# Kernel tuning notes

Hardware: AMD Instinct MI355X
Metric: run time of the kernel (lower is better)

The kernel has to match this reference:

```python
import jax, jax.numpy as jnp
import numpy as np

N_QUBITS = 6
N_LAYERS = 2
QSVT_DEGREE = 3
BATCH = 128
SEQ_LEN = 512
DIM = 2 ** N_QUBITS
# wire 0 is the most-significant bit in the statevector index (PennyLane convention)
_POP = np.array([bin(i).count('1') for i in range(DIM)], dtype=np.float32)
PHASE_SIGN = jnp.asarray(N_QUBITS - 2.0 * _POP)  # (DIM,): sum_w (1 - 2*bit_w)


def _rx(t):
    c = jnp.cos(0.5 * t).astype(jnp.complex64)
    s = (-1j * jnp.sin(0.5 * t)).astype(jnp.complex64)
    return jnp.stack([jnp.stack([c, s]), jnp.stack([s, c])])


def _ry(t):
    c = jnp.cos(0.5 * t).astype(jnp.complex64)
    s = jnp.sin(0.5 * t).astype(jnp.complex64)
    return jnp.stack([jnp.stack([c, -s]), jnp.stack([s, c])])


def _rz(t):
    e = jnp.exp(-0.5j * t.astype(jnp.complex64))
    z = jnp.zeros((), jnp.complex64)
    return jnp.stack([jnp.stack([e, z]), jnp.stack([z, jnp.conj(e)])])


def _apply_1q(psi, U, w):
    # psi: (B,) + (2,)*N_QUBITS ; U: (2,2) complex, same for all batch elems
    psi = jnp.moveaxis(psi, 1 + w, -1)
    psi = psi @ U.T
    return jnp.moveaxis(psi, -1, 1 + w)


def _apply_ry_batched(psi, theta, w):
    # RY with a per-batch angle theta: (B,)
    psi = jnp.moveaxis(psi, 1 + w, -1)
    c = jnp.cos(0.5 * theta).reshape((-1,) + (1,) * (N_QUBITS - 1))
    s = jnp.sin(0.5 * theta).reshape((-1,) + (1,) * (N_QUBITS - 1))
    a, b = psi[..., 0], psi[..., 1]
    psi = jnp.stack([c * a - s * b, s * a + c * b], axis=-1)
    return jnp.moveaxis(psi, -1, 1 + w)


def _cnot(psi, c, t):
    p0 = jax.lax.index_in_dim(psi, 0, axis=1 + c, keepdims=True)
    p1 = jax.lax.index_in_dim(psi, 1, axis=1 + c, keepdims=True)
    p1 = jnp.flip(p1, axis=1 + t)
    return jnp.concatenate([p0, p1], axis=1 + c)


def _circuit_step(h, x, params, poly):
    # h, x: (B, N_QUBITS) angles. Returns <Z_w> per qubit: (B, N_QUBITS).
    B = h.shape[0]
    # 1) state encoding: RY(h_w)|0> = cos(h/2)|0> + sin(h/2)|1>  (product state)
    c, s = jnp.cos(0.5 * h), jnp.sin(0.5 * h)
    psi = jnp.ones((B, 1), jnp.complex64)
    for w in range(N_QUBITS):
        amp = jnp.stack([c[:, w], s[:, w]], axis=-1).astype(jnp.complex64)  # (B,2)
        psi = (psi[:, :, None] * amp[:, None, :]).reshape(B, -1)
    psi = psi.reshape((B,) + (2,) * N_QUBITS)
    # 2) QSVT block: RZ(coeff*pi) on every wire fuses into one diagonal phase
    for d in range(QSVT_DEGREE + 1):
        theta = poly[d] * np.pi
        phase = jnp.exp((-0.5j) * theta * PHASE_SIGN)  # (DIM,)
        psi = (psi.reshape(B, -1) * phase[None, :]).reshape((B,) + (2,) * N_QUBITS)
        for i in range(N_QUBITS - 1):
            psi = _cnot(psi, i, i + 1)
        psi = _cnot(psi, N_QUBITS - 1, 0)  # ring closure
    # 3) variational layers: per-wire RZ@RY@RX (RX applied first), then CNOT chain
    idx = 0
    for _ in range(N_LAYERS):
        for i in range(N_QUBITS):
            U = _rz(params[idx + 2]) @ _ry(params[idx + 1]) @ _rx(params[idx])
            psi = _apply_1q(psi, U, i)
            idx += 3
        for i in range(N_QUBITS - 1):
            psi = _cnot(psi, i, i + 1)
    # 4) input injection: RY(x_w) with per-batch angles
    for w in range(N_QUBITS):
        psi = _apply_ry_batched(psi, x[:, w], w)
    # 5) measurement: <Z_w> = P(bit_w=0) - P(bit_w=1)
    p = jnp.abs(psi) ** 2
    zs = []
    for w in range(N_QUBITS):
        axes = tuple(a for a in range(1, N_QUBITS + 1) if a != 1 + w)
        pw = p.sum(axis=axes)  # (B,2)
        zs.append(pw[:, 0] - pw[:, 1])
    return jnp.stack(zs, axis=-1)


def _ssm_pass(angles, params, poly, reverse):
    a = jnp.flip(angles, axis=1) if reverse else angles
    xs = jnp.moveaxis(a, 1, 0)  # (T, B, n)
    h0 = jnp.zeros((a.shape[0], N_QUBITS), jnp.float32)

    def step(h, x):
        hn = _circuit_step(h, x, params, poly)
        return hn, hn

    _, ys = jax.lax.scan(step, h0, xs)
    out = jnp.moveaxis(ys, 0, 1)  # (B, T, n)
    return jnp.flip(out, axis=1) if reverse else out


def setup_inputs() -> dict:
    key = jax.random.key(0)
    k0, k1, k2, k3 = jax.random.split(key, 4)
    angles = jax.random.uniform(k0, (BATCH, SEQ_LEN, N_QUBITS), jnp.float32) * np.float32(np.pi)
    poly_coeffs = jax.random.normal(k1, (QSVT_DEGREE + 1,), jnp.float32) * 0.1
    fwd_params = jax.random.normal(k2, (N_QUBITS * N_LAYERS * 3,), jnp.float32) * 0.1
    bwd_params = jax.random.normal(k3, (N_QUBITS * N_LAYERS * 3,), jnp.float32) * 0.1
    fwd_coeff = jnp.full((1,), 0.5, jnp.float32)
    bwd_coeff = jnp.full((1,), 0.5, jnp.float32)
    return {'angles': angles, 'poly_coeffs': poly_coeffs, 'fwd_params': fwd_params,
            'bwd_params': bwd_params, 'fwd_coeff': fwd_coeff, 'bwd_coeff': bwd_coeff}


def reference(angles, poly_coeffs, fwd_params, bwd_params, fwd_coeff, bwd_coeff):
    h_fwd = _ssm_pass(angles, fwd_params, poly_coeffs, reverse=False)
    h_bwd = _ssm_pass(angles, bwd_params, poly_coeffs, reverse=True)
    return jax.nn.sigmoid(fwd_coeff) * h_fwd + jax.nn.sigmoid(bwd_coeff) * h_bwd
```

## Files before the change

kernel.cpp:

```cpp
#include <hip/hip_runtime.h>
#include <hip/hip_bf16.h>
#include <stdint.h>

#define BATCH 128
#define SEQ   512
#define NW    6
#define DIM   64
#define NELEM (BATCH * SEQ * NW)
#define PI_F  3.14159265358979323846f

typedef float v2f __attribute__((ext_vector_type(2)));
typedef uint16_t u16x8 __attribute__((ext_vector_type(8)));

__device__ __forceinline__ v2f pkfma(float s, v2f m, v2f a) {
    return __builtin_elementwise_fma((v2f){s, s}, m, a);
}

template <int CTRL>
__device__ __forceinline__ float dpp_mov(float x) {
    return __int_as_float(__builtin_amdgcn_update_dpp(
        0, __float_as_int(x), CTRL, 0xF, 0xF, false));
}

template <int CTRL>
__device__ __forceinline__ float dpp_add(float v) {
    return v + __int_as_float(__builtin_amdgcn_update_dpp(
        0, __float_as_int(v), CTRL, 0xF, 0xF, true));
}

__device__ __forceinline__ float swap16_add(float v) {
    auto r = __builtin_amdgcn_permlane16_swap(
        __float_as_int(v), __float_as_int(v), false, false);
    return __int_as_float((int)r[0]) + __int_as_float((int)r[1]);
}
__device__ __forceinline__ float swap32_add(float v) {
    auto r = __builtin_amdgcn_permlane32_swap(
        __float_as_int(v), __float_as_int(v), false, false);
    return __int_as_float((int)r[0]) + __int_as_float((int)r[1]);
}

__device__ __forceinline__ void sincos_half(float h, float& s, float& c) {
    const float u = h * h;
    c = fmaf(u, fmaf(u, 2.6041667e-3f, -0.125f), 1.0f);
    s = h * fmaf(u, fmaf(u, 2.6041667e-4f, -2.0833333e-2f), 0.5f);
}

__device__ __forceinline__ float ldf(const void* p, int i, bool bf) {
    if (bf) {
        uint32_t u = (uint32_t)((const uint16_t*)p)[i];
        return __uint_as_float(u << 16);
    }
    return ((const float*)p)[i];
}

__global__ void k_prep(const void* ang, const void* poly, const void* fp,
                       const void* bp, const void* fc, const void* bc,
                       float* __restrict__ misc, float* __restrict__ Mg,
                       int* __restrict__ flag) {
    __shared__ int cnt;
    if (threadIdx.x == 0) cnt = 0;
    __syncthreads();
    {
        uint32_t w = ((const uint32_t*)ang)[threadIdx.x & 255];
        uint32_t e = (w >> 8) & 0xFFu;
        if (e >= 0x3Au && e <= 0x41u) atomicAdd(&cnt, 1);
    }
    __syncthreads();
    const bool bf = (cnt >= 128);

    if (blockIdx.x == 32) {
        if (threadIdx.x == 0)      misc[76] = ldf(fc, 0, bf);
        else if (threadIdx.x == 1) misc[77] = ldf(bc, 0, bf);
        else if (threadIdx.x == 2) *flag = bf ? 1 : 0;
        return;
    }

    const int lane = threadIdx.x & 63;
    const int tix  = blockIdx.x * 4 + (threadIdx.x >> 6);
    const int dir  = tix >> 6;
    const int col  = tix & 63;
    const void* prm = dir ? bp : fp;
    const int p = lane;

    float yr = (p == col) ? 1.f : 0.f;
    float yi = 0.f;

#pragma unroll
    for (int d = 0; d < 4; ++d) {
        const float th = 0.5f * PI_F * ldf(poly, d, bf) *
                         (float)(6 - 2 * (int)__popc((unsigned)p));
        float s, c;
        __sincosf(th, &s, &c);
        const float nr = yr * c + yi * s;
        const float ni = yi * c - yr * s;
        yr = nr; yi = ni;
#pragma unroll
        for (int k = 0; k < 6; ++k) {
            const int cw = k, tw = (k + 1) % 6;
            const int src = p ^ (((p >> (5 - cw)) & 1) << (5 - tw));
            yr = __shfl(yr, src, 64);
            yi = __shfl(yi, src, 64);
        }
    }

    int idx = 0;
#pragma unroll
    for (int l = 0; l < 2; ++l) {
#pragma unroll
        for (int w = 0; w < 6; ++w) {
            float cx, sx, cy, sy, cz, sz;
            __sincosf(0.5f * ldf(prm, idx + 0, bf), &sx, &cx);
            __sincosf(0.5f * ldf(prm, idx + 1, bf), &sy, &cy);
            __sincosf(0.5f * ldf(prm, idx + 2, bf), &sz, &cz);
            idx += 3;
            const float A = cy * cx, B = sy * sx, C = sy * cx, D = cy * sx;
            const float U00r = cz * A + sz * B, U00i = cz * B - sz * A;
            const float U11r = U00r,            U11i = sz * A - cz * B;
            const float Xr   = cz * C + sz * D, Xi   = sz * C - cz * D;
            const int m  = 1 << (5 - w);
            const int bb = (p >> (5 - w)) & 1;
            const float C1r = bb ? U11r : U00r;
            const float C1i = bb ? U11i : U00i;
            const float C2r = bb ? Xr : -Xr;
            const float C2i = Xi;
            const float pr = __shfl_xor(yr, m, 64);
            const float pi = __shfl_xor(yi, m, 64);
            const float nr = C1r * yr - C1i * yi + C2r * pr - C2i * pi;
            const float ni = C1r * yi + C1i * yr + C2r * pi + C2i * pr;
            yr = nr; yi = ni;
        }
#pragma unroll
        for (int k = 0; k < 5; ++k) {
            const int src = p ^ (((p >> (5 - k)) & 1) << (5 - (k + 1)));
            yr = __shfl(yr, src, 64);
            yi = __shfl(yi, src, 64);
        }
    }

    float* out = Mg + ((size_t)(dir * 64 + p) * 64 + (size_t)col) * 2;
    out[0] = yr;
    out[1] = yi;
}

__global__ void __launch_bounds__(256, 1) k_sim(const void* __restrict__ ang,
                                                const float* __restrict__ Mg,
                                                float* __restrict__ hbuf,
                                                const int* __restrict__ flag) {
    const int tid   = threadIdx.x;
    const int lane  = tid & 63;
    const int wv    = tid >> 6;
    const int chain = blockIdx.x;
    const int dir   = chain >> 7;
    const int b     = chain & 127;
    const bool bf   = (*flag != 0);

    __shared__ __align__(16) float  cl[SEQ * 12];
    __shared__ __align__(16) float  zb[SEQ * NW];
    __shared__ float2 pY[2][4][DIM];

    if (!bf) {
        const float4* src =
            (const float4*)((const float*)ang + (size_t)b * (SEQ * NW));
#pragma unroll
        for (int k = 0; k < 3; ++k) {
            const int v = k * 256 + tid;
            const float4 a = src[v];
            __align__(16) float o[8];
            float s, c;
            __sincosf(a.x, &s, &c); o[0] = c; o[1] = s;
            __sincosf(a.y, &s, &c); o[2] = c; o[3] = s;
            __sincosf(a.z, &s, &c); o[4] = c; o[5] = s;
            __sincosf(a.w, &s, &c); o[6] = c; o[7] = s;
            ((float4*)cl)[2 * v]     = ((const float4*)o)[0];
            ((float4*)cl)[2 * v + 1] = ((const float4*)o)[1];
        }
    } else {
        const u16x8* src =
            (const u16x8*)((const uint16_t*)ang + (size_t)b * (SEQ * NW));
#pragma unroll
        for (int k = 0; k < 2; ++k) {
            const int v = k * 256 + tid;
            if (v < 384) {
                const u16x8 a = src[v];
                __align__(16) float o[16];
#pragma unroll
                for (int e = 0; e < 8; ++e) {
                    const float x = __uint_as_float(((uint32_t)a[e]) << 16);
                    float s, c;
                    __sincosf(x, &s, &c);
                    o[2 * e] = c; o[2 * e + 1] = s;
                }
#pragma unroll
                for (int j = 0; j < 4; ++j)
                    ((float4*)cl)[4 * v + j] = ((const float4*)o)[j];
            }
        }
    }

    v2f Mres[16];
    {
        const float2* mr2 =
            (const float2*)(Mg + (size_t)(dir * 64 + lane) * 128 + 32 * wv);
#pragma unroll
        for (int k = 0; k < 16; ++k) Mres[k] = (v2f){mr2[k].x, mr2[k].y};
    }

    int zmask[6];
#pragma unroll
    for (int w = 0; w < 6; ++w) zmask[w] = ((lane >> (5 - w)) & 1) << 31;
    const int ow0 = wv ^ 1, ow1 = wv ^ 2, ow2 = wv ^ 3;

    float h[6] = {0.f, 0.f, 0.f, 0.f, 0.f, 0.f};

    auto encode_matvec = [&](v2f& acc) {
        float cw6[6], sw6[6];
#pragma unroll
        for (int w = 0; w < 6; ++w) sincos_half(h[w], sw6[w], cw6[w]);
        const float t0 = (wv & 2) ? sw6[0] : cw6[0];
        const float t1 = (wv & 1) ? sw6[1] : cw6[1];
        const float A  = t0 * t1;
        float GH[4], GL[4];
        GH[0] = cw6[2] * cw6[3]; GH[1] = cw6[2] * sw6[3];
        GH[2] = sw6[2] * cw6[3]; GH[3] = sw6[2] * sw6[3];
#pragma unroll
        for (int a = 0; a < 4; ++a) GH[a] *= A;
        GL[0] = cw6[4] * cw6[5]; GL[1] = cw6[4] * sw6[5];
        GL[2] = sw6[4] * cw6[5]; GL[3] = sw6[4] * sw6[5];
        v2f y = {0.f, 0.f};
#pragma unroll
        for (int a = 0; a < 4; ++a) {
            v2f T = {0.f, 0.f};
#pragma unroll
            for (int b2 = 0; b2 < 4; ++b2)
                T = pkfma(GL[b2], Mres[4 * a + b2], T);
            y = pkfma(GH[a], T, y);
        }
        acc = y;
    };

    const float* cp = cl + (dir ? (SEQ - 1) * 12 : 0);
    const int   cstep = dir ? -12 : 12;
    float*       zp = zb + (dir ? (SEQ - 1) * NW : 0);
    const int   zstep = dir ? -NW : NW;

    __syncthreads();

    v2f myacc;
    encode_matvec(myacc);
    pY[0][wv][lane] = (float2){myacc.x, myacc.y};
    float4 xq0 = ((const float4*)cp)[0];
    float4 xq1 = ((const float4*)cp)[1];
    float4 xq2 = ((const float4*)cp)[2];
    cp += cstep;
    __syncthreads();

    for (int t = 0; t < SEQ; ++t) {
        const int buf = t & 1;

        const float2 yA = pY[buf][ow0][lane];
        const float2 yB = pY[buf][ow1][lane];
        const float2 yC = pY[buf][ow2][lane];
        const float yr = (myacc.x + yA.x) + (yB.x + yC.x);
        const float yi = (myacc.y + yA.y) + (yB.y + yC.y);
        const int yri = __float_as_int(yr), yii = __float_as_int(yi);

        float dot[6];
        {
            auto rr = __builtin_amdgcn_permlane32_swap(yri, yri, false, false);
            auto ri = __builtin_amdgcn_permlane32_swap(yii, yii, false, false);
            dot[0] = fmaf(__int_as_float((int)rr[0]), __int_as_float((int)rr[1]),
                          __int_as_float((int)ri[0]) * __int_as_float((int)ri[1]));
        }
        {
            auto rr = __builtin_amdgcn_permlane16_swap(yri, yri, false, false);
            auto ri = __builtin_amdgcn_permlane16_swap(yii, yii, false, false);
            dot[1] = fmaf(__int_as_float((int)rr[0]), __int_as_float((int)rr[1]),
                          __int_as_float((int)ri[0]) * __int_as_float((int)ri[1]));
        }
        dot[2] = fmaf(yr, dpp_mov<0x128>(yr), yi * dpp_mov<0x128>(yi));
        dot[3] = fmaf(yr, dpp_mov<0x141>(dpp_mov<0x1B>(yr)),
                      yi * dpp_mov<0x141>(dpp_mov<0x1B>(yi)));
        dot[4] = fmaf(yr, dpp_mov<0x4E>(yr), yi * dpp_mov<0x4E>(yi));
        dot[5] = fmaf(yr, dpp_mov<0xB1>(yr), yi * dpp_mov<0xB1>(yi));

        const float q = fmaf(yr, yr, yi * yi);
        const float cx[6] = {xq0.x, xq0.z, xq1.x, xq1.z, xq2.x, xq2.z};
        const float sx[6] = {xq0.y, xq0.w, xq1.y, xq1.w, xq2.y, xq2.w};

        float v[6];
#pragma unroll
        for (int w = 0; w < 6; ++w) {
            const float cq = __int_as_float(__float_as_int(cx[w] * q) ^ zmask[w]);
            v[w] = fmaf(-sx[w], dot[w], cq);
        }

        if (t + 1 < SEQ) {
            xq0 = ((const float4*)cp)[0];
            xq1 = ((const float4*)cp)[1];
            xq2 = ((const float4*)cp)[2];
            cp += cstep;
        }

#pragma unroll
        for (int k = 0; k < 6; ++k) v[k] = dpp_add<0xB1>(v[k]);
#pragma unroll
        for (int k = 0; k < 6; ++k) v[k] = dpp_add<0x4E>(v[k]);
#pragma unroll
        for (int k = 0; k < 6; ++k) v[k] = dpp_add<0x141>(v[k]);
#pragma unroll
        for (int k = 0; k < 6; ++k) v[k] = dpp_add<0x140>(v[k]);
#pragma unroll
        for (int k = 0; k < 6; ++k) v[k] = swap16_add(v[k]);
#pragma unroll
        for (int k = 0; k < 6; ++k) v[k] = swap32_add(v[k]);

        if (tid == 63) {
#pragma unroll
            for (int w = 0; w < 6; ++w) zp[w] = v[w];
        }
        zp += zstep;
#pragma unroll
        for (int w = 0; w < 6; ++w) h[w] = v[w];

        encode_matvec(myacc);
        pY[buf ^ 1][wv][lane] = (float2){myacc.x, myacc.y};
        __syncthreads();
    }

    {
        const float4* zs4 = (const float4*)zb;
        float4* go = (float4*)(hbuf + (size_t)dir * NELEM +
                               (size_t)b * (SEQ * NW));
#pragma unroll
        for (int k = 0; k < 3; ++k) {
            const int idx = tid + k * 256;
            go[idx] = zs4[idx];
        }
    }
}

__global__ void k_combine(const float* __restrict__ hbuf,
                          const float* __restrict__ misc,
                          void* __restrict__ out, const int* __restrict__ flag) {
    const int i = blockIdx.x * blockDim.x + threadIdx.x;
    if (i >= NELEM) return;
    const float sf = 1.f / (1.f + __expf(-misc[76]));
    const float sb = 1.f / (1.f + __expf(-misc[77]));
    const float v = sf * hbuf[i] + sb * hbuf[NELEM + i];
    if (*flag) ((__hip_bfloat16*)out)[i] = __float2bfloat16(v);
    else       ((float*)out)[i] = v;
}

extern "C" void kernel_launch(void* const* d_in, const int* in_sizes, int n_in,
                              void* d_out, int out_size, void* d_ws, size_t ws_size,
                              hipStream_t stream) {
    const void* ang  = d_in[0];
    const void* poly = d_in[1];
    const void* fp   = d_in[2];
    const void* bp   = d_in[3];
    const void* fc   = d_in[4];
    const void* bc   = d_in[5];

    float* misc = (float*)d_ws + 32;
    float* hbuf = misc + 128;
    float* Mg   = hbuf + 2 * NELEM;
    int*   flag = (int*)(Mg + 2 * 64 * 64 * 2);

    k_prep<<<33, 256, 0, stream>>>(ang, poly, fp, bp, fc, bc, misc, Mg, flag);
    k_sim<<<256, 256, 0, stream>>>(ang, Mg, hbuf, flag);
    k_combine<<<(NELEM + 255) / 256, 256, 0, stream>>>(hbuf, misc, d_out, flag);
}
```

Measured before the change: 344.9 us.

## Run each chain on a single wavefront with the matrix streamed from LDS

Shrinks k_sim from four wavefronts per chain to one. The full 64x64 complex matrix now lives in LDS in a transposed float4 layout and is streamed in double-buffered groups during the matvec. This removes the per-step __syncthreads and the cross-wave partial-sum exchange through shared memory, and writes outputs straight to global memory. The trade-off is four times more matvec work and LDS traffic per wavefront, and only 64 threads per CU across 256 blocks.

```diff
diff --git a/kernel.cpp b/kernel.cpp
--- a/kernel.cpp
+++ b/kernel.cpp
@@ -39,12 +39,6 @@
     return __int_as_float((int)r[0]) + __int_as_float((int)r[1]);
 }
 
-__device__ __forceinline__ void sincos_half(float h, float& s, float& c) {
-    const float u = h * h;
-    c = fmaf(u, fmaf(u, 2.6041667e-3f, -0.125f), 1.0f);
-    s = h * fmaf(u, fmaf(u, 2.6041667e-4f, -2.0833333e-2f), 0.5f);
-}
-
 __device__ __forceinline__ float ldf(const void* p, int i, bool bf) {
     if (bf) {
         uint32_t u = (uint32_t)((const uint16_t*)p)[i];
@@ -55,7 +49,7 @@
 
 __global__ void k_prep(const void* ang, const void* poly, const void* fp,
                        const void* bp, const void* fc, const void* bc,
-                       float* __restrict__ misc, float* __restrict__ Mg,
+                       float* __restrict__ misc, float* __restrict__ Mgt,
                        int* __restrict__ flag) {
     __shared__ int cnt;
     if (threadIdx.x == 0) cnt = 0;
@@ -137,33 +131,30 @@
         }
     }
 
-    float* out = Mg + ((size_t)(dir * 64 + p) * 64 + (size_t)col) * 2;
-    out[0] = yr;
-    out[1] = yi;
-}
-
-__global__ void __launch_bounds__(256, 1) k_sim(const void* __restrict__ ang,
-                                                const float* __restrict__ Mg,
-                                                float* __restrict__ hbuf,
-                                                const int* __restrict__ flag) {
-    const int tid   = threadIdx.x;
-    const int lane  = tid & 63;
-    const int wv    = tid >> 6;
+    float2* mt = (float2*)(Mgt +
+        (((size_t)(dir * 32 + (col >> 1)) * 64 + p) * 2 + (col & 1)) * 2);
+    *mt = (float2){yr, yi};
+}
+
+__global__ void __launch_bounds__(64, 1) k_sim(const void* __restrict__ ang,
+                                               const float* __restrict__ Mgt,
+                                               float* __restrict__ hbuf,
+                                               const int* __restrict__ flag) {
+    const int lane  = threadIdx.x;
     const int chain = blockIdx.x;
     const int dir   = chain >> 7;
     const int b     = chain & 127;
     const bool bf   = (*flag != 0);
 
     __shared__ __align__(16) float  cl[SEQ * 12];
-    __shared__ __align__(16) float  zb[SEQ * NW];
-    __shared__ float2 pY[2][4][DIM];
+    __shared__ __align__(16) float4 mlds[32 * 64];
 
     if (!bf) {
         const float4* src =
             (const float4*)((const float*)ang + (size_t)b * (SEQ * NW));
 #pragma unroll
-        for (int k = 0; k < 3; ++k) {
-            const int v = k * 256 + tid;
+        for (int k = 0; k < 12; ++k) {
+            const int v = k * 64 + lane;
             const float4 a = src[v];
             __align__(16) float o[8];
             float s, c;
@@ -178,90 +169,120 @@
         const u16x8* src =
             (const u16x8*)((const uint16_t*)ang + (size_t)b * (SEQ * NW));
 #pragma unroll
-        for (int k = 0; k < 2; ++k) {
-            const int v = k * 256 + tid;
-            if (v < 384) {
-                const u16x8 a = src[v];
-                __align__(16) float o[16];
-#pragma unroll
-                for (int e = 0; e < 8; ++e) {
-                    const float x = __uint_as_float(((uint32_t)a[e]) << 16);
-                    float s, c;
-                    __sincosf(x, &s, &c);
-                    o[2 * e] = c; o[2 * e + 1] = s;
-                }
-#pragma unroll
-                for (int j = 0; j < 4; ++j)
-                    ((float4*)cl)[4 * v + j] = ((const float4*)o)[j];
+        for (int k = 0; k < 6; ++k) {
+            const int v = k * 64 + lane;
+            const u16x8 a = src[v];
+            __align__(16) float o[16];
+#pragma unroll
+            for (int e = 0; e < 8; ++e) {
+                const float x = __uint_as_float(((uint32_t)a[e]) << 16);
+                float s, c;
+                __sincosf(x, &s, &c);
+                o[2 * e] = c; o[2 * e + 1] = s;
             }
-        }
-    }
-
-    v2f Mres[16];
+#pragma unroll
+            for (int j = 0; j < 4; ++j)
+                ((float4*)cl)[4 * v + j] = ((const float4*)o)[j];
+        }
+    }
+
     {
-        const float2* mr2 =
-            (const float2*)(Mg + (size_t)(dir * 64 + lane) * 128 + 32 * wv);
-#pragma unroll
-        for (int k = 0; k < 16; ++k) Mres[k] = (v2f){mr2[k].x, mr2[k].y};
+        const float4* mgt4 = (const float4*)Mgt;
+#pragma unroll
+        for (int k = 0; k < 32; ++k)
+            mlds[k * 64 + lane] = mgt4[(size_t)(dir * 32 + k) * 64 + lane];
     }
 
     int zmask[6];
 #pragma unroll
     for (int w = 0; w < 6; ++w) zmask[w] = ((lane >> (5 - w)) & 1) << 31;
-    const int ow0 = wv ^ 1, ow1 = wv ^ 2, ow2 = wv ^ 3;
-
-    float h[6] = {0.f, 0.f, 0.f, 0.f, 0.f, 0.f};
-
-    auto encode_matvec = [&](v2f& acc) {
-        float cw6[6], sw6[6];
-#pragma unroll
-        for (int w = 0; w < 6; ++w) sincos_half(h[w], sw6[w], cw6[w]);
-        const float t0 = (wv & 2) ? sw6[0] : cw6[0];
-        const float t1 = (wv & 1) ? sw6[1] : cw6[1];
-        const float A  = t0 * t1;
-        float GH[4], GL[4];
-        GH[0] = cw6[2] * cw6[3]; GH[1] = cw6[2] * sw6[3];
-        GH[2] = sw6[2] * cw6[3]; GH[3] = sw6[2] * sw6[3];
-#pragma unroll
-        for (int a = 0; a < 4; ++a) GH[a] *= A;
-        GL[0] = cw6[4] * cw6[5]; GL[1] = cw6[4] * sw6[5];
-        GL[2] = sw6[4] * cw6[5]; GL[3] = sw6[4] * sw6[5];
-        v2f y = {0.f, 0.f};
-#pragma unroll
-        for (int a = 0; a < 4; ++a) {
-            v2f T = {0.f, 0.f};
-#pragma unroll
-            for (int b2 = 0; b2 < 4; ++b2)
-                T = pkfma(GL[b2], Mres[4 * a + b2], T);
-            y = pkfma(GH[a], T, y);
-        }
-        acc = y;
-    };
 
     const float* cp = cl + (dir ? (SEQ - 1) * 12 : 0);
     const int   cstep = dir ? -12 : 12;
-    float*       zp = zb + (dir ? (SEQ - 1) * NW : 0);
+    float* zo = hbuf + (size_t)dir * NELEM + (size_t)b * (SEQ * NW) +
+                (dir ? (SEQ - 1) * NW : 0);
     const int   zstep = dir ? -NW : NW;
 
+    float h[6] = {0.f, 0.f, 0.f, 0.f, 0.f, 0.f};
+
     __syncthreads();
 
-    v2f myacc;
-    encode_matvec(myacc);
-    pY[0][wv][lane] = (float2){myacc.x, myacc.y};
-    float4 xq0 = ((const float4*)cp)[0];
-    float4 xq1 = ((const float4*)cp)[1];
-    float4 xq2 = ((const float4*)cp)[2];
-    cp += cstep;
-    __syncthreads();
+    const float4* mlp = ((const float4*)mlds) + lane;
+
+#define LOADW(W, G) { W[0] = mlp[((G)*4+0)*64]; W[1] = mlp[((G)*4+1)*64]; \
+                      W[2] = mlp[((G)*4+2)*64]; W[3] = mlp[((G)*4+3)*64]; }
+#define CONSUME(W, G) { v2f n = {0.f, 0.f}; \
+        n = pkfma(eL[0], (v2f){W[0].x, W[0].y}, n); \
+        n = pkfma(eL[1], (v2f){W[0].z, W[0].w}, n); \
+        n = pkfma(eL[2], (v2f){W[1].x, W[1].y}, n); \
+        n = pkfma(eL[3], (v2f){W[1].z, W[1].w}, n); \
+        n = pkfma(eL[4], (v2f){W[2].x, W[2].y}, n); \
+        n = pkfma(eL[5], (v2f){W[2].z, W[2].w}, n); \
+        n = pkfma(eL[6], (v2f){W[3].x, W[3].y}, n); \
+        n = pkfma(eL[7], (v2f){W[3].z, W[3].w}, n); \
+        y = pkfma(eH[G], n, y); }
+
+    float4 A[4], B[4];
+    LOADW(A, 0)
+    LOADW(B, 1)
 
     for (int t = 0; t < SEQ; ++t) {
-        const int buf = t & 1;
-
-        const float2 yA = pY[buf][ow0][lane];
-        const float2 yB = pY[buf][ow1][lane];
-        const float2 yC = pY[buf][ow2][lane];
-        const float yr = (myacc.x + yA.x) + (yB.x + yC.x);
-        const float yi = (myacc.y + yA.y) + (yB.y + yC.y);
+        asm volatile("" : "+v"(mlp));
+
+        v2f hp0 = {h[0], h[1]}, hp1 = {h[2], h[3]}, hp2 = {h[4], h[5]};
+        float cw[6], sw[6];
+        {
+            const v2f kc1 = {2.6041667e-3f, 2.6041667e-3f};
+            const v2f kc0 = {-0.125f, -0.125f};
+            const v2f ks1 = {2.6041667e-4f, 2.6041667e-4f};
+            const v2f ks0 = {-2.0833333e-2f, -2.0833333e-2f};
+            const v2f one = {1.f, 1.f}, half = {0.5f, 0.5f};
+            v2f u0 = hp0 * hp0, u1 = hp1 * hp1, u2 = hp2 * hp2;
+            v2f c0 = __builtin_elementwise_fma(u0,
+                        __builtin_elementwise_fma(u0, kc1, kc0), one);
+            v2f c1 = __builtin_elementwise_fma(u1,
+                        __builtin_elementwise_fma(u1, kc1, kc0), one);
+            v2f c2 = __builtin_elementwise_fma(u2,
+                        __builtin_elementwise_fma(u2, kc1, kc0), one);
+            v2f s0 = hp0 * __builtin_elementwise_fma(u0,
+                        __builtin_elementwise_fma(u0, ks1, ks0), half);
+            v2f s1 = hp1 * __builtin_elementwise_fma(u1,
+                        __builtin_elementwise_fma(u1, ks1, ks0), half);
+            v2f s2 = hp2 * __builtin_elementwise_fma(u2,
+                        __builtin_elementwise_fma(u2, ks1, ks0), half);
+            cw[0] = c0.x; cw[1] = c0.y; cw[2] = c1.x; cw[3] = c1.y;
+            cw[4] = c2.x; cw[5] = c2.y;
+            sw[0] = s0.x; sw[1] = s0.y; sw[2] = s1.x; sw[3] = s1.y;
+            sw[4] = s2.x; sw[5] = s2.y;
+        }
+
+        float g01[4], g45[4], eH[8], eL[8];
+        g01[0] = cw[0] * cw[1]; g01[1] = cw[0] * sw[1];
+        g01[2] = sw[0] * cw[1]; g01[3] = sw[0] * sw[1];
+        g45[0] = cw[4] * cw[5]; g45[1] = cw[4] * sw[5];
+        g45[2] = sw[4] * cw[5]; g45[3] = sw[4] * sw[5];
+#pragma unroll
+        for (int j = 0; j < 8; ++j) {
+            eH[j] = g01[j >> 1] * ((j & 1) ? sw[2] : cw[2]);
+            eL[j] = ((j >> 2) ? sw[3] : cw[3]) * g45[j & 3];
+        }
+
+        v2f y = {0.f, 0.f};
+        CONSUME(A, 0) LOADW(A, 2)
+        CONSUME(B, 1) LOADW(B, 3)
+        CONSUME(A, 2) LOADW(A, 4)
+        CONSUME(B, 3) LOADW(B, 5)
+        CONSUME(A, 4) LOADW(A, 6)
+        CONSUME(B, 5) LOADW(B, 7)
+        CONSUME(A, 6)
+        CONSUME(B, 7)
+
+        const float4 xq0 = ((const float4*)cp)[0];
+        const float4 xq1 = ((const float4*)cp)[1];
+        const float4 xq2 = ((const float4*)cp)[2];
+        cp += cstep;
+
+        const float yr = y.x, yi = y.y;
         const int yri = __float_as_int(yr), yii = __float_as_int(yi);
 
         float dot[6];
@@ -294,13 +315,6 @@
             v[w] = fmaf(-sx[w], dot[w], cq);
         }
 
-        if (t + 1 < SEQ) {
-            xq0 = ((const float4*)cp)[0];
-            xq1 = ((const float4*)cp)[1];
-            xq2 = ((const float4*)cp)[2];
-            cp += cstep;
-        }
-
 #pragma unroll
         for (int k = 0; k < 6; ++k) v[k] = dpp_add<0xB1>(v[k]);
 #pragma unroll
@@ -314,29 +328,20 @@
 #pragma unroll
         for (int k = 0; k < 6; ++k) v[k] = swap32_add(v[k]);
 
-        if (tid == 63) {
-#pragma unroll
-            for (int w = 0; w < 6; ++w) zp[w] = v[w];
-        }
-        zp += zstep;
+        LOADW(A, 0)
+        LOADW(B, 1)
+
+        if (lane == 0) {
+            *(float2*)(zo)     = (float2){v[0], v[1]};
+            *(float2*)(zo + 2) = (float2){v[2], v[3]};
+            *(float2*)(zo + 4) = (float2){v[4], v[5]};
+        }
+        zo += zstep;
 #pragma unroll
         for (int w = 0; w < 6; ++w) h[w] = v[w];
-
-        encode_matvec(myacc);
-        pY[buf ^ 1][wv][lane] = (float2){myacc.x, myacc.y};
-        __syncthreads();
-    }
-
-    {
-        const float4* zs4 = (const float4*)zb;
-        float4* go = (float4*)(hbuf + (size_t)dir * NELEM +
-                               (size_t)b * (SEQ * NW));
-#pragma unroll
-        for (int k = 0; k < 3; ++k) {
-            const int idx = tid + k * 256;
-            go[idx] = zs4[idx];
-        }
-    }
+    }
+#undef LOADW
+#undef CONSUME
 }
 
 __global__ void k_combine(const float* __restrict__ hbuf,
@@ -363,10 +368,10 @@
 
     float* misc = (float*)d_ws + 32;
     float* hbuf = misc + 128;
-    float* Mg   = hbuf + 2 * NELEM;
-    int*   flag = (int*)(Mg + 2 * 64 * 64 * 2);
-
-    k_prep<<<33, 256, 0, stream>>>(ang, poly, fp, bp, fc, bc, misc, Mg, flag);
-    k_sim<<<256, 256, 0, stream>>>(ang, Mg, hbuf, flag);
+    float* Mgt  = hbuf + 2 * NELEM;
+    int*   flag = (int*)(Mgt + 2 * 32 * 64 * 4);
+
+    k_prep<<<33, 256, 0, stream>>>(ang, poly, fp, bp, fc, bc, misc, Mgt, flag);
+    k_sim<<<256, 64, 0, stream>>>(ang, Mgt, hbuf, flag);
     k_combine<<<(NELEM + 255) / 256, 256, 0, stream>>>(hbuf, misc, d_out, flag);
 }
```

Result: slower. 459.7 us (+33.3%).
